# Kernel optimization log

Measured on AMD Instinct MI355X. Metric: run time of the kernel, lower is better.

The kernel has to match this reference:

```python
import jax, jax.numpy as jnp
import numpy as np

HIDDEN = 1024
HEADS = 16
HEAD_DIM = HIDDEN // HEADS


def setup_inputs() -> dict:
    key = jax.random.key(0)
    kx, kw = jax.random.split(key)
    x = jax.random.normal(kx, (1, 4096, HIDDEN), dtype=jnp.float32)
    # torch Linear weight is [out, in]; we store as [in, out] for x @ W
    W_qkv = jax.random.normal(kw, (HIDDEN, 3 * HIDDEN), dtype=jnp.float32) * (HIDDEN ** -0.5)
    return {"x": x, "W_qkv": W_qkv}


def reference(x, W_qkv):
    B, T, _ = x.shape
    qkv = x @ W_qkv                                    # [B, T, 3*HIDDEN]
    qkv = qkv.reshape(B, T, 3, HEADS, HEAD_DIM)
    qkv = jnp.transpose(qkv, (2, 0, 3, 1, 4))          # [3, B, H, T, Dh]
    q, k, v = qkv[0], qkv[1], qkv[2]
    scale = HEAD_DIM ** -0.5
    attn = jnp.einsum("bhqd,bhkd->bhqk", q, k) * scale  # [B, H, T, T] materialized (naive)
    attn = jax.nn.softmax(attn, axis=-1)
    out = jnp.einsum("bhqk,bhkd->bhqd", attn, v)        # [B, H, T, Dh]
    out = jnp.transpose(out, (0, 2, 1, 3)).reshape(B, T, HIDDEN)
    return out
```

## Files before the change

### kernel.cpp

```cpp
#include <hip/hip_runtime.h>

#define SEQ 4096
#define HID 1024
#define NH  16
#define DH  64
#define N3  3072

typedef __attribute__((ext_vector_type(4))) float floatx4;
typedef __attribute__((ext_vector_type(8))) short shortx8;
typedef __attribute__((ext_vector_type(4))) short shortx4;

__device__ __forceinline__ short f2bf(float f) {
    return (short)((__builtin_bit_cast(unsigned, f) + 0x8000u) >> 16);
}
__device__ __forceinline__ unsigned pk2bf(float a, float b) {
    unsigned ua = __builtin_bit_cast(unsigned, a) + 0x8000u;
    unsigned ub = __builtin_bit_cast(unsigned, b) + 0x8000u;
    return (ua >> 16) | (ub & 0xFFFF0000u);
}
__device__ __forceinline__ shortx4 pk4bf(float a, float b, float c, float d) {
    union { unsigned u[2]; shortx4 s; } x;
    x.u[0] = pk2bf(a, b);
    x.u[1] = pk2bf(c, d);
    return x.s;
}

__device__ __forceinline__ unsigned cvtpk(float lo, float hi) {
    unsigned r;
    asm("v_cvt_pk_bf16_f32 %0, %1, %2" : "=v"(r) : "v"(lo), "v"(hi));
    return r;
}

#if __has_builtin(__builtin_amdgcn_exp2f)
#define fexp2 __builtin_amdgcn_exp2f
#else
#define fexp2 exp2f
#endif

#define mfma32 __builtin_amdgcn_mfma_f32_16x16x32_bf16

__device__ __forceinline__ void gll16(const short* g, short* l) {
    __builtin_amdgcn_global_load_lds(
        (const __attribute__((address_space(1))) unsigned*)g,
        (__attribute__((address_space(3))) unsigned*)l, 16, 0, 0);
}

__global__ __launch_bounds__(256) void convert_x(
    const float* __restrict__ x, short* __restrict__ Xb)
{
    size_t i = (size_t)blockIdx.x * 256 + threadIdx.x;
    float4 v = *(const float4*)&x[i * 4];
    shortx4 b = pk4bf(v.x, v.y, v.z, v.w);
    *(shortx4*)&Xb[i * 4] = b;
}

__global__ __launch_bounds__(256) void transpose_W(
    const float* __restrict__ W, short* __restrict__ Wt)
{
    __shared__ short Ws[128 * 40];
    const int t  = threadIdx.x;
    const int n0 = blockIdx.x * 128;
    const int k0 = blockIdx.y * 32;
    #pragma unroll
    for (int i = 0; i < 4; i++) {
        int idx = t + i * 256;
        int k = idx >> 5, c4 = idx & 31;
        float4 v = *(const float4*)&W[(size_t)(k0 + k) * N3 + n0 + c4 * 4];
        Ws[(c4 * 4 + 0) * 40 + k] = f2bf(v.x);
        Ws[(c4 * 4 + 1) * 40 + k] = f2bf(v.y);
        Ws[(c4 * 4 + 2) * 40 + k] = f2bf(v.z);
        Ws[(c4 * 4 + 3) * 40 + k] = f2bf(v.w);
    }
    __syncthreads();
    #pragma unroll
    for (int i = 0; i < 2; i++) {
        int idx = t + i * 256;
        int n = idx >> 2, seg = idx & 3;
        shortx8 g = *(const shortx8*)&Ws[n * 40 + seg * 8];
        *(shortx8*)&Wt[(size_t)(n0 + n) * HID + k0 + seg * 8] = g;
    }
}

#define LDC 136
__global__ __launch_bounds__(256) void qkv_gemm(
    const short* __restrict__ Xb, const short* __restrict__ Wt,
    short* __restrict__ Qb, short* __restrict__ Kb, short* __restrict__ Vb)
{
    __shared__ short SM[18432];
    short* As = SM;
    short* Bs = SM + 128 * 64;
    const int tid  = threadIdx.x;
    const int m0   = blockIdx.x * 128;
    const int n0   = blockIdx.y * 128;
    const int lane = tid & 63;
    const int wid  = tid >> 6;
    const int wm   = (wid >> 1) * 64;
    const int wn   = (wid & 1) * 64;
    const int l15  = lane & 15;
    const int quad = lane >> 4;

    floatx4 acc[4][4];
    #pragma unroll
    for (int i = 0; i < 4; i++)
        #pragma unroll
        for (int j = 0; j < 4; j++)
            acc[i][j] = (floatx4){0.f, 0.f, 0.f, 0.f};

    const int arow = tid >> 3, ac = tid & 7;
    const int swk  = (ac ^ (arow & 7)) << 3;
    const short* ag = Xb + (size_t)(m0 + arow) * HID + swk;
    const short* bg = Wt + (size_t)(n0 + arow) * HID + swk;
    short* al = As + (size_t)(tid & 192) * 8;
    short* bl = Bs + (size_t)(tid & 192) * 8;
    const int r7 = l15 & 7;

    for (int k0 = 0; k0 < HID; k0 += 64) {
        #pragma unroll
        for (int i = 0; i < 4; i++)
            gll16(ag + (size_t)i * 32 * HID + k0, al + i * 2048);
        #pragma unroll
        for (int i = 0; i < 4; i++)
            gll16(bg + (size_t)i * 32 * HID + k0, bl + i * 2048);
        __syncthreads();
        #pragma unroll
        for (int kh = 0; kh < 2; kh++) {
            shortx8 af[4], bf[4];
            #pragma unroll
            for (int t = 0; t < 4; t++) {
                int R = wm + t * 16 + l15;
                af[t] = *(const shortx8*)&As[(R << 6) + ((((kh << 2) + quad) ^ r7) << 3)];
                int Rb = wn + t * 16 + l15;
                bf[t] = *(const shortx8*)&Bs[(Rb << 6) + ((((kh << 2) + quad) ^ r7) << 3)];
            }
            #pragma unroll
            for (int tm = 0; tm < 4; tm++)
                #pragma unroll
                for (int tn = 0; tn < 4; tn++)
                    acc[tm][tn] = mfma32(af[tm], bf[tn], acc[tm][tn], 0, 0, 0);
        }
        __syncthreads();
    }

    short* Cs = SM;
    const float sc = (n0 < 1024) ? 0.18033688011112042f : 1.0f;
    #pragma unroll
    for (int tm = 0; tm < 4; tm++)
        #pragma unroll
        for (int tn = 0; tn < 4; tn++)
            #pragma unroll
            for (int r = 0; r < 4; r++)
                Cs[(wm + tm * 16 + quad * 4 + r) * LDC + wn + tn * 16 + l15] =
                    f2bf(acc[tm][tn][r] * sc);
    __syncthreads();
    short* base = (n0 < 1024) ? Qb : (n0 < 2048 ? Kb : Vb);
    const int h0 = (n0 & 1023) >> 6;
    #pragma unroll
    for (int j = 0; j < 8; j++) {
        int idx = tid + j * 256;
        int row = idx >> 4, col = (idx & 15) * 8;
        shortx8 v = *(const shortx8*)&Cs[row * LDC + col];
        *(shortx8*)&base[((size_t)(h0 + (col >> 6)) * SEQ + m0 + row) * DH + (col & 63)] = v;
    }
}

__global__ __launch_bounds__(256) void transpose_V(
    const short* __restrict__ Vb, short* __restrict__ Vt)
{
    __shared__ short Ts[64 * 72];
    const int t  = threadIdx.x;
    const int t0 = blockIdx.x * 64;
    const int h  = blockIdx.y;
    #pragma unroll
    for (int i = 0; i < 2; i++) {
        int idx = t + i * 256;
        int r = idx >> 3, seg = idx & 7;
        shortx8 g = *(const shortx8*)&Vb[((size_t)h * SEQ + t0 + r) * DH + seg * 8];
        *(shortx8*)&Ts[r * 72 + seg * 8] = g;
    }
    __syncthreads();
    #pragma unroll
    for (int i = 0; i < 2; i++) {
        int idx = t + i * 256;
        int d = idx >> 3, tseg = idx & 7;
        shortx8 g;
        #pragma unroll
        for (int j = 0; j < 8; j++) g[j] = Ts[(tseg * 8 + j) * 72 + d];
        *(shortx8*)&Vt[((size_t)h * DH + d) * SEQ + t0 + tseg * 8] = g;
    }
}

__global__ __launch_bounds__(128, 2) void flash_attn(
    const short* __restrict__ Qb, const short* __restrict__ Kb,
    const short* __restrict__ Vt, float* __restrict__ out,
    float* __restrict__ Opart, float* __restrict__ Lpart,
    int kpc, int nit, int final)
{
    __shared__ short Ks[2][4096];
    __shared__ short Vs[2][4096];
    const int tid  = threadIdx.x;
    const int wid  = tid >> 6;
    const int lane = tid & 63;
    const int l15  = lane & 15;
    const int quad = lane >> 4;

    const int nblk = (int)(gridDim.x * gridDim.y * gridDim.z);
    const int lin  = (int)blockIdx.x + ((int)blockIdx.y << 5) + ((int)blockIdx.z << 9);
    const int work = (lin & 7) * (nblk >> 3) + (lin >> 3);
    const int h    = (work >> 5) & 15;
    const int ch   = work >> 9;
    const int q0   = (work & 31) * 128 + wid * 64;
    const int tstart = ch * kpc;
    const shortx8 ones8 = {(short)0x3F80, (short)0x3F80, (short)0x3F80, (short)0x3F80,
                           (short)0x3F80, (short)0x3F80, (short)0x3F80, (short)0x3F80};
    const floatx4 z4 = {0.f, 0.f, 0.f, 0.f};

    shortx8 qf[4][2];
    #pragma unroll
    for (int s = 0; s < 4; s++) {
        const short* qp = Qb + ((size_t)h * SEQ + q0 + s * 16 + l15) * DH;
        qf[s][0] = *(const shortx8*)(qp + quad * 8);
        qf[s][1] = *(const shortx8*)(qp + 32 + quad * 8);
    }

    floatx4 oacc[4][4];
    #pragma unroll
    for (int s = 0; s < 4; s++)
        #pragma unroll
        for (int dn = 0; dn < 4; dn++)
            oacc[s][dn] = z4;
    floatx4 lacc[4] = {z4, z4, z4, z4};

    const int rK   = tid >> 3, sK = tid & 7;
    const int key0 = 8 * ((rK >> 2) & 3) + (rK & 3);
    const int swo  = (sK ^ (rK & 7)) << 3;
    const short* kg = Kb + ((size_t)h * SEQ + tstart + key0) * DH + swo;
    const short* vg = Vt + ((size_t)h * DH + rK) * SEQ + tstart + swo;
    const int wbase = (tid & 64) * 8;

#define STAGE(b) do { \
        gll16(kg,            &Ks[b][wbase]); \
        gll16(kg + 4 * DH,   &Ks[b][wbase + 1024]); \
        gll16(kg + 32 * DH,  &Ks[b][wbase + 2048]); \
        gll16(kg + 36 * DH,  &Ks[b][wbase + 3072]); \
        gll16(vg,            &Vs[b][wbase]); \
        gll16(vg + 16 * SEQ, &Vs[b][wbase + 1024]); \
        gll16(vg + 32 * SEQ, &Vs[b][wbase + 2048]); \
        gll16(vg + 48 * SEQ, &Vs[b][wbase + 3072]); \
    } while (0)

    STAGE(0);
    kg += 64 * DH;  vg += 64;

    for (int it = 0; it < nit; it++) {
        __syncthreads();
        if (it + 1 < nit) {
            int b = (it + 1) & 1;
            STAGE(b);
            kg += 64 * DH;  vg += 64;
        }
        const short* ks = Ks[it & 1];
        const short* vs = Vs[it & 1];

        union { unsigned u[4]; shortx8 s8; } pa[4][2];
        #pragma unroll
        for (int pair = 0; pair < 2; pair++) {
            int Ra = (pair * 2) * 16 + l15;
            int Rb = (pair * 2 + 1) * 16 + l15;
            int offa = (Ra << 6) + ((quad ^ (Ra & 7)) << 3);
            int offb = (Rb << 6) + ((quad ^ (Rb & 7)) << 3);
            shortx8 kf0a = *(const shortx8*)&ks[offa];
            shortx8 kf1a = *(const shortx8*)&ks[offa ^ 32];
            shortx8 kf0b = *(const shortx8*)&ks[offb];
            shortx8 kf1b = *(const shortx8*)&ks[offb ^ 32];
            floatx4 sta[4], stb[4];
            __builtin_amdgcn_s_setprio(1);
            #pragma unroll
            for (int s = 0; s < 4; s++) {
                floatx4 a = mfma32(kf0a, qf[s][0], z4, 0, 0, 0);
                a = mfma32(kf1a, qf[s][1], a, 0, 0, 0);
                sta[s] = a;
                floatx4 b = mfma32(kf0b, qf[s][0], z4, 0, 0, 0);
                b = mfma32(kf1b, qf[s][1], b, 0, 0, 0);
                stb[s] = b;
            }
            __builtin_amdgcn_s_setprio(0);
            #pragma unroll
            for (int s = 0; s < 4; s++) {
                pa[s][pair].u[0] = cvtpk(fexp2(sta[s][0]), fexp2(sta[s][1]));
                pa[s][pair].u[1] = cvtpk(fexp2(sta[s][2]), fexp2(sta[s][3]));
                pa[s][pair].u[2] = cvtpk(fexp2(stb[s][0]), fexp2(stb[s][1]));
                pa[s][pair].u[3] = cvtpk(fexp2(stb[s][2]), fexp2(stb[s][3]));
            }
        }

        __builtin_amdgcn_s_setprio(1);
        #pragma unroll
        for (int s = 0; s < 4; s++) {
            lacc[s] = mfma32(pa[s][0].s8, ones8, lacc[s], 0, 0, 0);
            lacc[s] = mfma32(pa[s][1].s8, ones8, lacc[s], 0, 0, 0);
        }

        #pragma unroll
        for (int dn = 0; dn < 4; dn++) {
            int row = dn * 16 + l15;
            int off = (row << 6) + ((quad ^ (row & 7)) << 3);
            shortx8 va = *(const shortx8*)&vs[off];
            shortx8 vb = *(const shortx8*)&vs[off ^ 32];
            #pragma unroll
            for (int s = 0; s < 4; s++) {
                oacc[s][dn] = mfma32(pa[s][0].s8, va, oacc[s][dn], 0, 0, 0);
                oacc[s][dn] = mfma32(pa[s][1].s8, vb, oacc[s][dn], 0, 0, 0);
            }
        }
        __builtin_amdgcn_s_setprio(0);
    }
#undef STAGE

    if (final) {
        #pragma unroll
        for (int s = 0; s < 4; s++)
            #pragma unroll
            for (int r = 0; r < 4; r++) {
                float rl = 1.0f / lacc[s][r];
                int query = q0 + s * 16 + quad * 4 + r;
                float* d = out + (size_t)query * HID + h * DH + l15;
                #pragma unroll
                for (int dn = 0; dn < 4; dn++)
                    d[dn * 16] = oacc[s][dn][r] * rl;
            }
    } else {
        #pragma unroll
        for (int s = 0; s < 4; s++)
            #pragma unroll
            for (int r = 0; r < 4; r++) {
                int query = q0 + s * 16 + quad * 4 + r;
                float* d = Opart + ((size_t)ch * SEQ + query) * HID + h * DH + l15;
                #pragma unroll
                for (int dn = 0; dn < 4; dn++)
                    d[dn * 16] = oacc[s][dn][r];
            }
        if (l15 == 0) {
            float* lp = Lpart + ((size_t)ch * NH + h) * SEQ + q0;
            #pragma unroll
            for (int s = 0; s < 4; s++)
                #pragma unroll
                for (int r = 0; r < 4; r++)
                    lp[s * 16 + quad * 4 + r] = lacc[s][r];
        }
    }
}

__global__ __launch_bounds__(256) void combine(
    const float* __restrict__ Opart, const float* __restrict__ Lpart,
    float* __restrict__ out, int chn)
{
    size_t i = ((size_t)blockIdx.x * 256 + threadIdx.x) * 4;
    int q = (int)(i >> 10);
    int h = ((int)i & 1023) >> 6;
    float4 o = {0.f, 0.f, 0.f, 0.f};
    float l = 0.f;
    for (int c = 0; c < chn; c++) {
        float4 p = *(const float4*)&Opart[(size_t)c * SEQ * HID + i];
        o.x += p.x; o.y += p.y; o.z += p.z; o.w += p.w;
        l += Lpart[((size_t)c * NH + h) * SEQ + q];
    }
    float rl = 1.0f / l;
    float4 r = {o.x * rl, o.y * rl, o.z * rl, o.w * rl};
    *(float4*)&out[i] = r;
}

extern "C" void kernel_launch(void* const* d_in, const int* in_sizes, int n_in,
                              void* d_out, int out_size, void* d_ws, size_t ws_size,
                              hipStream_t stream) {
    const float* x = (const float*)d_in[0];
    const float* W = (const float*)d_in[1];
    float* out = (float*)d_out;

    short* Xb = (short*)d_ws;
    short* Wt = Xb + (size_t)SEQ * HID;
    short* Qb = Wt + (size_t)N3 * HID;
    short* Kb = Qb + (size_t)NH * SEQ * DH;
    short* Vb = Kb + (size_t)NH * SEQ * DH;
    short* Vt = Xb;
    float* Opart = (float*)(Vb + (size_t)NH * SEQ * DH);

    const size_t need = 39845888ull
                      + 2ull * SEQ * HID * 4
                      + 2ull * NH * SEQ * 4;
    const int chn = (ws_size >= need) ? 2 : 1;
    float* Lpart = Opart + (size_t)chn * SEQ * HID;
    const int kpc = SEQ / chn, nit = kpc / 64;

    convert_x  <<<dim3(SEQ * HID / 1024), 256, 0, stream>>>(x, Xb);
    transpose_W<<<dim3(N3 / 128, HID / 32), 256, 0, stream>>>(W, Wt);
    qkv_gemm   <<<dim3(SEQ / 128, N3 / 128), 256, 0, stream>>>(Xb, Wt, Qb, Kb, Vb);
    transpose_V<<<dim3(SEQ / 64, NH), 256, 0, stream>>>(Vb, Vt);
    flash_attn <<<dim3(SEQ / 128, NH, chn), 128, 0, stream>>>(
        Qb, Kb, Vt, out, Opart, Lpart, kpc, nit, chn == 1);
    if (chn > 1)
        combine<<<dim3(SEQ * HID / 1024), 256, 0, stream>>>(Opart, Lpart, out, chn);
}
```

Before: 202.6 us.

## Fuse V transpose into QKV GEMM epilogue, enlarge attention blocks, split keys four ways

The QKV GEMM epilogue now writes V already transposed, straight from shared memory, so the separate transpose_V kernel and its extra global round trip go away. Flash attention moves to 256-thread blocks covering 256 queries, so each staged K/V tile is shared by four waves and each thread issues fewer async loads. The P·V product is now interleaved per key-pair to shorten the live range of the P fragments. The key dimension can be split into four chunks when the workspace allows, which adds more partial-output traffic to the combine kernel.

```diff
diff --git a/kernel.cpp b/kernel.cpp
--- a/kernel.cpp
+++ b/kernel.cpp
@@ -84,7 +84,7 @@
 #define LDC 136
 __global__ __launch_bounds__(256) void qkv_gemm(
     const short* __restrict__ Xb, const short* __restrict__ Wt,
-    short* __restrict__ Qb, short* __restrict__ Kb, short* __restrict__ Vb)
+    short* __restrict__ Qb, short* __restrict__ Kb, short* __restrict__ Vt)
 {
     __shared__ short SM[18432];
     short* As = SM;
@@ -152,44 +152,31 @@
                 Cs[(wm + tm * 16 + quad * 4 + r) * LDC + wn + tn * 16 + l15] =
                     f2bf(acc[tm][tn][r] * sc);
     __syncthreads();
-    short* base = (n0 < 1024) ? Qb : (n0 < 2048 ? Kb : Vb);
     const int h0 = (n0 & 1023) >> 6;
-    #pragma unroll
-    for (int j = 0; j < 8; j++) {
-        int idx = tid + j * 256;
-        int row = idx >> 4, col = (idx & 15) * 8;
-        shortx8 v = *(const shortx8*)&Cs[row * LDC + col];
-        *(shortx8*)&base[((size_t)(h0 + (col >> 6)) * SEQ + m0 + row) * DH + (col & 63)] = v;
-    }
-}
-
-__global__ __launch_bounds__(256) void transpose_V(
-    const short* __restrict__ Vb, short* __restrict__ Vt)
-{
-    __shared__ short Ts[64 * 72];
-    const int t  = threadIdx.x;
-    const int t0 = blockIdx.x * 64;
-    const int h  = blockIdx.y;
-    #pragma unroll
-    for (int i = 0; i < 2; i++) {
-        int idx = t + i * 256;
-        int r = idx >> 3, seg = idx & 7;
-        shortx8 g = *(const shortx8*)&Vb[((size_t)h * SEQ + t0 + r) * DH + seg * 8];
-        *(shortx8*)&Ts[r * 72 + seg * 8] = g;
-    }
-    __syncthreads();
-    #pragma unroll
-    for (int i = 0; i < 2; i++) {
-        int idx = t + i * 256;
-        int d = idx >> 3, tseg = idx & 7;
-        shortx8 g;
-        #pragma unroll
-        for (int j = 0; j < 8; j++) g[j] = Ts[(tseg * 8 + j) * 72 + d];
-        *(shortx8*)&Vt[((size_t)h * DH + d) * SEQ + t0 + tseg * 8] = g;
-    }
-}
-
-__global__ __launch_bounds__(128, 2) void flash_attn(
+    if (n0 < 2048) {
+        short* base = (n0 < 1024) ? Qb : Kb;
+        #pragma unroll
+        for (int j = 0; j < 8; j++) {
+            int idx = tid + j * 256;
+            int row = idx >> 4, col = (idx & 15) * 8;
+            shortx8 v = *(const shortx8*)&Cs[row * LDC + col];
+            *(shortx8*)&base[((size_t)(h0 + (col >> 6)) * SEQ + m0 + row) * DH + (col & 63)] = v;
+        }
+    } else {
+        #pragma unroll
+        for (int j = 0; j < 8; j++) {
+            int idx = tid + j * 256;
+            int col = idx >> 4;
+            int t8  = (idx & 15) * 8;
+            shortx8 v;
+            #pragma unroll
+            for (int k = 0; k < 8; k++) v[k] = Cs[(t8 + k) * LDC + col];
+            *(shortx8*)&Vt[((size_t)(h0 + (col >> 6)) * DH + (col & 63)) * SEQ + m0 + t8] = v;
+        }
+    }
+}
+
+__global__ __launch_bounds__(256, 3) void flash_attn(
     const short* __restrict__ Qb, const short* __restrict__ Kb,
     const short* __restrict__ Vt, float* __restrict__ out,
     float* __restrict__ Opart, float* __restrict__ Lpart,
@@ -204,11 +191,11 @@
     const int quad = lane >> 4;
 
     const int nblk = (int)(gridDim.x * gridDim.y * gridDim.z);
-    const int lin  = (int)blockIdx.x + ((int)blockIdx.y << 5) + ((int)blockIdx.z << 9);
+    const int lin  = (int)blockIdx.x + ((int)blockIdx.y << 4) + ((int)blockIdx.z << 8);
     const int work = (lin & 7) * (nblk >> 3) + (lin >> 3);
-    const int h    = (work >> 5) & 15;
-    const int ch   = work >> 9;
-    const int q0   = (work & 31) * 128 + wid * 64;
+    const int h    = (work >> 4) & 15;
+    const int ch   = work >> 8;
+    const int q0   = (work & 15) * 256 + wid * 64;
     const int tstart = ch * kpc;
     const shortx8 ones8 = {(short)0x3F80, (short)0x3F80, (short)0x3F80, (short)0x3F80,
                            (short)0x3F80, (short)0x3F80, (short)0x3F80, (short)0x3F80};
@@ -231,21 +218,17 @@
     floatx4 lacc[4] = {z4, z4, z4, z4};
 
     const int rK   = tid >> 3, sK = tid & 7;
-    const int key0 = 8 * ((rK >> 2) & 3) + (rK & 3);
+    const int key0 = 8 * ((rK >> 2) & 3) + 4 * ((rK >> 4) & 1) + (rK & 3);
     const int swo  = (sK ^ (rK & 7)) << 3;
     const short* kg = Kb + ((size_t)h * SEQ + tstart + key0) * DH + swo;
     const short* vg = Vt + ((size_t)h * DH + rK) * SEQ + tstart + swo;
-    const int wbase = (tid & 64) * 8;
+    const int wslot = (tid & 192) * 8;
 
 #define STAGE(b) do { \
-        gll16(kg,            &Ks[b][wbase]); \
-        gll16(kg + 4 * DH,   &Ks[b][wbase + 1024]); \
-        gll16(kg + 32 * DH,  &Ks[b][wbase + 2048]); \
-        gll16(kg + 36 * DH,  &Ks[b][wbase + 3072]); \
-        gll16(vg,            &Vs[b][wbase]); \
-        gll16(vg + 16 * SEQ, &Vs[b][wbase + 1024]); \
-        gll16(vg + 32 * SEQ, &Vs[b][wbase + 2048]); \
-        gll16(vg + 48 * SEQ, &Vs[b][wbase + 3072]); \
+        gll16(kg,            &Ks[b][wslot]); \
+        gll16(kg + 32 * DH,  &Ks[b][wslot + 2048]); \
+        gll16(vg,            &Vs[b][wslot]); \
+        gll16(vg + 32 * SEQ, &Vs[b][wslot + 2048]); \
     } while (0)
 
     STAGE(0);
@@ -261,11 +244,10 @@
         const short* ks = Ks[it & 1];
         const short* vs = Vs[it & 1];
 
-        union { unsigned u[4]; shortx8 s8; } pa[4][2];
         #pragma unroll
         for (int pair = 0; pair < 2; pair++) {
             int Ra = (pair * 2) * 16 + l15;
-            int Rb = (pair * 2 + 1) * 16 + l15;
+            int Rb = Ra + 16;
             int offa = (Ra << 6) + ((quad ^ (Ra & 7)) << 3);
             int offb = (Rb << 6) + ((quad ^ (Rb & 7)) << 3);
             shortx8 kf0a = *(const shortx8*)&ks[offa];
@@ -284,35 +266,29 @@
                 stb[s] = b;
             }
             __builtin_amdgcn_s_setprio(0);
+            union { unsigned u[4]; shortx8 s8; } pa[4];
             #pragma unroll
             for (int s = 0; s < 4; s++) {
-                pa[s][pair].u[0] = cvtpk(fexp2(sta[s][0]), fexp2(sta[s][1]));
-                pa[s][pair].u[1] = cvtpk(fexp2(sta[s][2]), fexp2(sta[s][3]));
-                pa[s][pair].u[2] = cvtpk(fexp2(stb[s][0]), fexp2(stb[s][1]));
-                pa[s][pair].u[3] = cvtpk(fexp2(stb[s][2]), fexp2(stb[s][3]));
-            }
-        }
-
-        __builtin_amdgcn_s_setprio(1);
-        #pragma unroll
-        for (int s = 0; s < 4; s++) {
-            lacc[s] = mfma32(pa[s][0].s8, ones8, lacc[s], 0, 0, 0);
-            lacc[s] = mfma32(pa[s][1].s8, ones8, lacc[s], 0, 0, 0);
-        }
-
-        #pragma unroll
-        for (int dn = 0; dn < 4; dn++) {
-            int row = dn * 16 + l15;
-            int off = (row << 6) + ((quad ^ (row & 7)) << 3);
-            shortx8 va = *(const shortx8*)&vs[off];
-            shortx8 vb = *(const shortx8*)&vs[off ^ 32];
-            #pragma unroll
-            for (int s = 0; s < 4; s++) {
-                oacc[s][dn] = mfma32(pa[s][0].s8, va, oacc[s][dn], 0, 0, 0);
-                oacc[s][dn] = mfma32(pa[s][1].s8, vb, oacc[s][dn], 0, 0, 0);
-            }
-        }
-        __builtin_amdgcn_s_setprio(0);
+                pa[s].u[0] = cvtpk(fexp2(sta[s][0]), fexp2(sta[s][1]));
+                pa[s].u[1] = cvtpk(fexp2(sta[s][2]), fexp2(sta[s][3]));
+                pa[s].u[2] = cvtpk(fexp2(stb[s][0]), fexp2(stb[s][1]));
+                pa[s].u[3] = cvtpk(fexp2(stb[s][2]), fexp2(stb[s][3]));
+            }
+            __builtin_amdgcn_s_setprio(1);
+            #pragma unroll
+            for (int s = 0; s < 4; s++)
+                lacc[s] = mfma32(pa[s].s8, ones8, lacc[s], 0, 0, 0);
+            #pragma unroll
+            for (int dn = 0; dn < 4; dn++) {
+                int row = dn * 16 + l15;
+                int off = ((row << 6) + ((quad ^ (row & 7)) << 3)) ^ (pair << 5);
+                shortx8 vv = *(const shortx8*)&vs[off];
+                #pragma unroll
+                for (int s = 0; s < 4; s++)
+                    oacc[s][dn] = mfma32(pa[s].s8, vv, oacc[s][dn], 0, 0, 0);
+            }
+            __builtin_amdgcn_s_setprio(0);
+        }
     }
 #undef STAGE
 
@@ -380,22 +356,21 @@
     short* Wt = Xb + (size_t)SEQ * HID;
     short* Qb = Wt + (size_t)N3 * HID;
     short* Kb = Qb + (size_t)NH * SEQ * DH;
-    short* Vb = Kb + (size_t)NH * SEQ * DH;
-    short* Vt = Xb;
-    float* Opart = (float*)(Vb + (size_t)NH * SEQ * DH);
-
-    const size_t need = 39845888ull
-                      + 2ull * SEQ * HID * 4
-                      + 2ull * NH * SEQ * 4;
-    const int chn = (ws_size >= need) ? 2 : 1;
+    short* Vt = Kb + (size_t)NH * SEQ * DH;
+    float* Opart = (float*)(Vt + (size_t)NH * SEQ * DH);
+
+    const size_t need4 = 39845888ull
+                       + 4ull * SEQ * HID * 4
+                       + 4ull * NH * SEQ * 4;
+    const size_t need2 = 39845888ull + 2ull * SEQ * HID * 4 + 2ull * NH * SEQ * 4;
+    const int chn = (ws_size >= need4) ? 4 : ((ws_size >= need2) ? 2 : 1);
     float* Lpart = Opart + (size_t)chn * SEQ * HID;
     const int kpc = SEQ / chn, nit = kpc / 64;
 
     convert_x  <<<dim3(SEQ * HID / 1024), 256, 0, stream>>>(x, Xb);
     transpose_W<<<dim3(N3 / 128, HID / 32), 256, 0, stream>>>(W, Wt);
-    qkv_gemm   <<<dim3(SEQ / 128, N3 / 128), 256, 0, stream>>>(Xb, Wt, Qb, Kb, Vb);
-    transpose_V<<<dim3(SEQ / 64, NH), 256, 0, stream>>>(Vb, Vt);
-    flash_attn <<<dim3(SEQ / 128, NH, chn), 128, 0, stream>>>(
+    qkv_gemm   <<<dim3(SEQ / 128, N3 / 128), 256, 0, stream>>>(Xb, Wt, Qb, Kb, Vt);
+    flash_attn <<<dim3(SEQ / 256, NH, chn), 256, 0, stream>>>(
         Qb, Kb, Vt, out, Opart, Lpart, kpc, nit, chn == 1);
     if (chn > 1)
         combine<<<dim3(SEQ * HID / 1024), 256, 0, stream>>>(Opart, Lpart, out, chn);
```

After: 201.5 us. No clear change (-0.5%).
